# Optimization experiments

Measured on AMD Instinct MI355X. Metric: run time of the kernel, lower is better.

Reference implementation:

```python
import jax, jax.numpy as jnp
import numpy as np

B, T, D, H = 4, 1024, 1024, 16
DH = D // H
NEG_BIG = jnp.float32(-2.0**32 + 1)


def layer_norm(x, scale, bias, eps=1e-5):
    mean = jnp.mean(x, axis=-1, keepdims=True)
    var = jnp.mean(jnp.square(x - mean), axis=-1, keepdims=True)
    return (x - mean) * jax.lax.rsqrt(var + eps) * scale + bias


def setup_inputs() -> dict:
    key = jax.random.key(0)
    ks = jax.random.split(key, 10)
    s = 0.02
    x = jax.random.normal(ks[0], (B, T, D), jnp.float32)
    mask = jax.random.randint(ks[1], (B, T), 0, 2).astype(jnp.float32)
    return {
        "x": x,
        "mask": mask,
        "wq": jax.random.normal(ks[2], (D, D), jnp.float32) * s,
        "wk": jax.random.normal(ks[3], (D, D), jnp.float32) * s,
        "wv": jax.random.normal(ks[4], (D, D), jnp.float32) * s,
        "w1": jax.random.normal(ks[5], (D, D), jnp.float32) * s,
        "b1": jnp.zeros((D,), jnp.float32),
        "w2": jax.random.normal(ks[6], (D, D), jnp.float32) * s,
        "b2": jnp.zeros((D,), jnp.float32),
        "ln1_s": jnp.ones((D,), jnp.float32),
        "ln1_b": jnp.zeros((D,), jnp.float32),
        "ln2_s": jnp.ones((D,), jnp.float32),
        "ln2_b": jnp.zeros((D,), jnp.float32),
        "ln3_s": jnp.ones((D,), jnp.float32),
        "ln3_b": jnp.zeros((D,), jnp.float32),
    }


def _mask_enc(x, mask, wq, wk, wv, w1, b1, w2, b2,
              ln1_s, ln1_b, ln2_s, ln2_b, ln3_s, ln3_b):
    b, t, d = x.shape
    # --- multi-head attention (hand-rolled, matches torch split/cat trick) ---
    Q = (x @ wq).reshape(b, t, H, DH).transpose(0, 2, 1, 3)  # [B,H,T,dh]
    K = (x @ wk).reshape(b, t, H, DH).transpose(0, 2, 1, 3)
    V = (x @ wv).reshape(b, t, H, DH).transpose(0, 2, 1, 3)
    scores = jnp.einsum('bhqd,bhkd->bhqk', Q, K) / jnp.sqrt(jnp.float32(DH))
    # key padding mask from sign of |K| row sums
    key_m = jnp.sign(jnp.sum(jnp.abs(K), axis=-1))  # [B,H,T]
    scores = jnp.where(key_m[:, :, None, :] == 0, NEG_BIG, scores)
    # FORWARD direction: allowed where col_index > row_index (strict)
    idx = jnp.arange(t)
    allowed = (idx[None, :] > idx[:, None]).astype(scores.dtype)  # [T,T]
    scores = scores + (1.0 - allowed) * (-10000.0)
    attn = jax.nn.softmax(scores, axis=-1)
    # post-softmax query mask multiply
    query_m = jnp.sign(jnp.sum(jnp.abs(Q), axis=-1))[:, :, :, None]  # [B,H,T,1]
    attn = attn * query_m
    out = jnp.einsum('bhqk,bhkd->bhqd', attn, V)
    out = out.transpose(0, 2, 1, 3).reshape(b, t, d)  # combine heads
    out = out * mask[:, :, None]
    # --- residual + layernorm wrapper (attention) ---
    h1 = layer_norm(x + out, ln1_s, ln1_b)
    # --- FFN + residual + layernorm ---
    ffn = jax.nn.relu(h1 @ w1 + b1) @ w2 + b2
    h2 = layer_norm(h1 + ffn, ln2_s, ln2_b)
    # --- output normalization ---
    return layer_norm(h2, ln3_s, ln3_b)


def reference(x, mask, wq, wk, wv, w1, b1, w2, b2,
              ln1_s, ln1_b, ln2_s, ln2_b, ln3_s, ln3_b):
    return _mask_enc(x, mask, wq, wk, wv, w1, b1, w2, b2,
                     ln1_s, ln1_b, ln2_s, ln2_b, ln3_s, ln3_b)
```

## Files before the change

### kernel.cpp

```cpp
#include <hip/hip_runtime.h>
#include <stdint.h>


#define B_  4
#define T_  1024
#define D_  1024
#define H_  16
#define DH_ 64

typedef __attribute__((ext_vector_type(8))) short short8;
typedef __attribute__((ext_vector_type(4))) float floatx4;
typedef __attribute__((ext_vector_type(4))) _Float16 half4;

__device__ __forceinline__ unsigned short f2bf(float f) {
  union { float f; uint32_t u; } a; a.f = f;
  uint32_t r = a.u + 0x7FFFu + ((a.u >> 16) & 1u);
  return (unsigned short)(r >> 16);
}
__device__ __forceinline__ float bf2f(unsigned short u) {
  union { uint32_t u; float f; } a; a.u = ((uint32_t)u) << 16;
  return a.f;
}

#define GLD_LDS16(g, l) __builtin_amdgcn_global_load_lds( \
    (const __attribute__((address_space(1))) unsigned int*)(g), \
    (__attribute__((address_space(3))) unsigned int*)(l), 16, 0, 0)

__global__ __launch_bounds__(256)
void prep_kernel(const float4* __restrict__ x4, unsigned short* __restrict__ xb,
                 const float* __restrict__ w0, const float* __restrict__ w1,
                 const float* __restrict__ w2, const float* __restrict__ w3,
                 const float* __restrict__ w4, unsigned short* __restrict__ dst_all) {
  const int t = threadIdx.x;
  if (blockIdx.x < 4096) {
    int idx = blockIdx.x * 256 + t;
    float4 v = x4[idx];
    union { uint2 u; unsigned short s[4]; } o;
    o.s[0] = f2bf(v.x); o.s[1] = f2bf(v.y); o.s[2] = f2bf(v.z); o.s[3] = f2bf(v.w);
    *(uint2*)&xb[(size_t)idx * 4] = o.u;
    return;
  }
  const int b = blockIdx.x - 4096;
  const int z = b >> 8, ky = (b >> 4) & 15, nx = b & 15;
  const float* src = (z == 0) ? w0 : (z == 1) ? w1 : (z == 2) ? w2 : (z == 3) ? w3 : w4;
  unsigned short* dst = dst_all + (size_t)z * D_ * D_;
  __shared__ __align__(16) unsigned short tile[64 * 72];
  const int k0 = ky * 64, n0 = nx * 64;
#pragma unroll
  for (int c = 0; c < 4; ++c) {
    int idx = c * 256 + t;
    int r = idx >> 4, cc = (idx & 15) << 2;
    float4 v = *(const float4*)&src[(size_t)(k0 + r) * D_ + n0 + cc];
    tile[(cc + 0) * 72 + r] = f2bf(v.x);
    tile[(cc + 1) * 72 + r] = f2bf(v.y);
    tile[(cc + 2) * 72 + r] = f2bf(v.z);
    tile[(cc + 3) * 72 + r] = f2bf(v.w);
  }
  __syncthreads();
  int rr = t >> 2, ck = (t & 3) << 4;
  uint4 v0 = *(const uint4*)&tile[rr * 72 + ck];
  uint4 v1 = *(const uint4*)&tile[rr * 72 + ck + 8];
  *(uint4*)&dst[(size_t)(n0 + rr) * D_ + k0 + ck] = v0;
  *(uint4*)&dst[(size_t)(n0 + rr) * D_ + k0 + ck + 8] = v1;
}

__global__ __launch_bounds__(256, 2)
void gemm_qkv(const unsigned short* __restrict__ A,
              const unsigned short* __restrict__ Bt,
              unsigned short* __restrict__ oQ, unsigned short* __restrict__ oK,
              _Float16* __restrict__ oV) {
  const int K = 1024;
  __shared__ __align__(16) unsigned short As[128 * 32];
  __shared__ __align__(16) unsigned short Bs[128 * 32];
  __shared__ __align__(16) _Float16 Cs[2 * 64 * 136];
  const int t = threadIdx.x;
  const int lane = t & 63, w = t >> 6;
  const int quad = lane >> 4, lm = lane & 15;
  const int wm = w >> 1, wn = w & 1;
  const int m0 = blockIdx.y * 128, n0 = blockIdx.x * 128;
  const int arow = w * 32 + (lane >> 2), acol = (lane & 3) << 3;

  floatx4 acc[4][4];
#pragma unroll
  for (int i = 0; i < 4; ++i)
#pragma unroll
    for (int j = 0; j < 4; ++j) acc[i][j] = (floatx4){0.f, 0.f, 0.f, 0.f};

  for (int kt = 0; kt < K; kt += 32) {
    const unsigned short* ga = A + (size_t)(m0 + arow) * K + kt + acol;
    const unsigned short* gb = Bt + (size_t)(n0 + arow) * K + kt + acol;
    GLD_LDS16(ga, &As[(w * 32) * 32]);
    GLD_LDS16(ga + (size_t)16 * K, &As[(w * 32 + 16) * 32]);
    GLD_LDS16(gb, &Bs[(w * 32) * 32]);
    GLD_LDS16(gb + (size_t)16 * K, &Bs[(w * 32 + 16) * 32]);
    __syncthreads();
    short8 a[4], b[4];
#pragma unroll
    for (int i = 0; i < 4; ++i) a[i] = *(const short8*)&As[(wm * 64 + i * 16 + lm) * 32 + quad * 8];
#pragma unroll
    for (int j = 0; j < 4; ++j) b[j] = *(const short8*)&Bs[(wn * 64 + j * 16 + lm) * 32 + quad * 8];
#pragma unroll
    for (int i = 0; i < 4; ++i)
#pragma unroll
      for (int j = 0; j < 4; ++j)
        acc[i][j] = __builtin_amdgcn_mfma_f32_16x16x32_bf16(a[i], b[j], acc[i][j], 0, 0, 0);
    __syncthreads();
  }

  if (n0 < 2048) {
    unsigned short* p = (n0 < 1024) ? oQ : oK;
    const float qscale = (n0 < 1024) ? 0.18033688f : 1.0f;
#pragma unroll
    for (int i = 0; i < 4; ++i) {
      int gmb = m0 + wm * 64 + i * 16 + quad * 4;
#pragma unroll
      for (int j = 0; j < 4; ++j) {
        int gn = n0 + wn * 64 + j * 16 + lm;
        int nn = gn & 1023, hh = nn >> 6, dd = nn & 63;
#pragma unroll
        for (int r = 0; r < 4; ++r) {
          int gm = gmb + r;
          int bb = gm >> 10, tt = gm & 1023;
          p[(((size_t)bb * H_ + hh) * T_ + tt) * DH_ + dd] = f2bf(acc[i][j][r] * qscale);
        }
      }
    }
  } else {
#pragma unroll
    for (int i = 0; i < 4; ++i) {
#pragma unroll
      for (int j = 0; j < 4; ++j) {
        int gn = n0 + wn * 64 + j * 16 + lm;
        int hd = (gn >> 6) & 1, dd = gn & 63;
        int kperm = quad * 32 + (wm * 4 + i) * 4;
        union { _Float16 h[4]; uint2 u; } pk;
#pragma unroll
        for (int r = 0; r < 4; ++r) pk.h[r] = (_Float16)acc[i][j][r];
        *(uint2*)&Cs[((size_t)(hd * 64 + dd)) * 136 + kperm] = pk.u;
      }
    }
    __syncthreads();
    const int row = t >> 1, half = t & 1;
    const int hd = row >> 6, dd = row & 63;
    const int hh = ((n0 & 1023) >> 6) + hd;
    const int bb = m0 >> 10, kbg = (m0 >> 7) & 7;
    const _Float16* srcp = &Cs[(size_t)(hd * 64 + dd) * 136 + half * 64];
    _Float16* dstp = oV + ((((size_t)bb * H_ + hh) * DH_ + dd) * 8 + kbg) * 128 + half * 64;
#pragma unroll
    for (int g = 0; g < 8; ++g)
      *(uint4*)(dstp + g * 8) = *(const uint4*)(srcp + g * 8);
  }
}

template <int MODE>
__global__ __launch_bounds__(256, 2)
void gemm_ffn(const unsigned short* __restrict__ A,
              const unsigned short* __restrict__ Bt,
              unsigned short* __restrict__ oBf, float* __restrict__ oF,
              const float* __restrict__ bias) {
  const int K = 1024, N = 1024;
  __shared__ __align__(16) unsigned short As[64 * 32];
  __shared__ __align__(16) unsigned short Bs[128 * 32];
  const int t = threadIdx.x;
  const int lane = t & 63, w = t >> 6;
  const int quad = lane >> 4, lm = lane & 15;
  const int wm = w >> 1, wn = w & 1;
  const int m0 = blockIdx.y * 64, n0 = blockIdx.x * 128;
  const int lrow = lane >> 2, lcol = (lane & 3) << 3;

  floatx4 acc[2][4];
#pragma unroll
  for (int i = 0; i < 2; ++i)
#pragma unroll
    for (int j = 0; j < 4; ++j) acc[i][j] = (floatx4){0.f, 0.f, 0.f, 0.f};

  for (int kt = 0; kt < K; kt += 32) {
    const unsigned short* ga = A + (size_t)(m0 + w * 16 + lrow) * K + kt + lcol;
    const unsigned short* gb = Bt + (size_t)(n0 + w * 32 + lrow) * K + kt + lcol;
    GLD_LDS16(ga, &As[(w * 16) * 32]);
    GLD_LDS16(gb, &Bs[(w * 32) * 32]);
    GLD_LDS16(gb + (size_t)16 * K, &Bs[(w * 32 + 16) * 32]);
    __syncthreads();
    short8 a[2], b[4];
#pragma unroll
    for (int i = 0; i < 2; ++i) a[i] = *(const short8*)&As[(wm * 32 + i * 16 + lm) * 32 + quad * 8];
#pragma unroll
    for (int j = 0; j < 4; ++j) b[j] = *(const short8*)&Bs[(wn * 64 + j * 16 + lm) * 32 + quad * 8];
#pragma unroll
    for (int i = 0; i < 2; ++i)
#pragma unroll
      for (int j = 0; j < 4; ++j)
        acc[i][j] = __builtin_amdgcn_mfma_f32_16x16x32_bf16(a[i], b[j], acc[i][j], 0, 0, 0);
    __syncthreads();
  }

#pragma unroll
  for (int i = 0; i < 2; ++i) {
    int gmb = m0 + wm * 32 + i * 16 + quad * 4;
#pragma unroll
    for (int j = 0; j < 4; ++j) {
      int gn = n0 + wn * 64 + j * 16 + lm;
      float bv = bias[gn];
#pragma unroll
      for (int r = 0; r < 4; ++r) {
        int gm = gmb + r;
        float v = acc[i][j][r] + bv;
        if (MODE == 1) {
          oBf[(size_t)gm * N + gn] = f2bf(fmaxf(v, 0.f));
        } else {
          oF[(size_t)gm * N + gn] = v;
        }
      }
    }
  }
}

__global__ __launch_bounds__(256)
void flash_attn(const unsigned short* __restrict__ Qb,
                const unsigned short* __restrict__ Kb,
                const _Float16* __restrict__ Vtg,
                const float* __restrict__ maskp,
                unsigned short* __restrict__ attn) {
  __shared__ __align__(16) unsigned short KLs[2][8192];
  __shared__ __align__(16) _Float16      VLs[2][8192];

  const int t = threadIdx.x;
  const int lane = t & 63, w = t >> 6;
  const int quad = lane >> 4, lm = lane & 15;

  const int bid = blockIdx.x;
  const int hi  = bid >> 8;
  const int lo  = bid & 255;
  const int xcd = lo & 7;
  const int hgrp = (lo >> 3) & 7;
  const int qpair = lo >> 6;
  const int qb = hi ? (7 - qpair) : qpair;
  const int head = hgrp * 8 + xcd;
  const int hh = head & 15, bb = head >> 4;
  const int q0 = qb << 7;

  const size_t headoff = ((size_t)bb * H_ + hh) * T_ * DH_;
  const unsigned short* Qh = Qb + headoff;
  const unsigned short* Kh = Kb + headoff;
  const _Float16* Vh = Vtg + headoff;

  short8 qf[2][2];
#pragma unroll
  for (int qg = 0; qg < 2; ++qg)
#pragma unroll
    for (int ks = 0; ks < 2; ++ks)
      qf[qg][ks] = *(const short8*)(Qh + (size_t)(q0 + w * 32 + qg * 16 + lm) * 64 + ks * 32 + quad * 8);

  float lsum[2] = {0.f, 0.f};
  floatx4 acc[2][4];
#pragma unroll
  for (int qg = 0; qg < 2; ++qg)
#pragma unroll
    for (int j2 = 0; j2 < 4; ++j2) acc[qg][j2] = (floatx4){0.f, 0.f, 0.f, 0.f};

  const int qglob0 = q0 + w * 32 + lm;
  const bool excl1 = (qglob0 + 16 == 1023);
  const float MSHIFT = 14426.950408f;

  const int my_lo  = (qb == 7 && w == 3) ? 0 : qb;
  const int blk_lo = (qb == 7) ? 0 : qb;

  const unsigned short* gk[4];
  const _Float16* gv[4];
#pragma unroll
  for (int i = 0; i < 4; ++i) {
    int s = w * 4 + i;
    gk[i] = Kh + (size_t)((s >> 1) * 16 + lm) * 64 + (s & 1) * 32 + quad * 8;
    gv[i] = Vh + ((size_t)((s >> 2) * 16 + lm) * 8) * 128 + quad * 32 + (s & 3) * 8;
  }

#pragma unroll
  for (int i = 0; i < 4; ++i) {
    int s = w * 4 + i;
    GLD_LDS16(gk[i] + (size_t)blk_lo * 8192, &KLs[0][s * 512]);
    GLD_LDS16(gv[i] + (size_t)blk_lo * 128,  &VLs[0][s * 512]);
  }

  int cur = 0;
  for (int kb = blk_lo; kb < 8; ++kb) {
    __syncthreads();
    if (kb + 1 < 8) {
      int nxt = cur ^ 1;
#pragma unroll
      for (int i = 0; i < 4; ++i) {
        int s = w * 4 + i;
        GLD_LDS16(gk[i] + (size_t)(kb + 1) * 8192, &KLs[nxt][s * 512]);
        GLD_LDS16(gv[i] + (size_t)(kb + 1) * 128,  &VLs[nxt][s * 512]);
      }
    }
    if (kb >= my_lo) {
      const unsigned short* Kc = &KLs[cur][0];
      const _Float16* Vc = &VLs[cur][0];
      const int k0 = kb * 128;
      const bool need_mask = (kb <= qb);

      short8 kA = *(const short8*)&Kc[(0 * 64 + lane) * 8];
      short8 kB = *(const short8*)&Kc[(1 * 64 + lane) * 8];
      half4 vA0 = *(const half4*)&Vc[((0 * 4 + 0) * 64 + lane) * 8];
      half4 vA1 = *(const half4*)&Vc[((1 * 4 + 0) * 64 + lane) * 8];
      half4 vA2 = *(const half4*)&Vc[((2 * 4 + 0) * 64 + lane) * 8];
      half4 vA3 = *(const half4*)&Vc[((3 * 4 + 0) * 64 + lane) * 8];

#pragma unroll
      for (int j = 0; j < 8; ++j) {
        short8 nA, nB; half4 n0, n1, n2, n3;
        if (j < 7) {
          int jn = j + 1;
          nA = *(const short8*)&Kc[((jn * 2 + 0) * 64 + lane) * 8];
          nB = *(const short8*)&Kc[((jn * 2 + 1) * 64 + lane) * 8];
          n0 = *(const half4*)&Vc[((0 * 4 + (jn >> 1)) * 64 + lane) * 8 + (jn & 1) * 4];
          n1 = *(const half4*)&Vc[((1 * 4 + (jn >> 1)) * 64 + lane) * 8 + (jn & 1) * 4];
          n2 = *(const half4*)&Vc[((2 * 4 + (jn >> 1)) * 64 + lane) * 8 + (jn & 1) * 4];
          n3 = *(const half4*)&Vc[((3 * 4 + (jn >> 1)) * 64 + lane) * 8 + (jn & 1) * 4];
        }
        floatx4 st[2];
#pragma unroll
        for (int qg = 0; qg < 2; ++qg) {
          floatx4 z = (floatx4){0.f, 0.f, 0.f, 0.f};
          z = __builtin_amdgcn_mfma_f32_16x16x32_bf16(kA, qf[qg][0], z, 0, 0, 0);
          st[qg] = __builtin_amdgcn_mfma_f32_16x16x32_bf16(kB, qf[qg][1], z, 0, 0, 0);
        }
        half4 pa[2];
#pragma unroll
        for (int qg = 0; qg < 2; ++qg) {
          const int qq = qglob0 + qg * 16;
          const bool skip = (qg == 1) && excl1;
#pragma unroll
          for (int r = 0; r < 4; ++r) {
            int kg = k0 + j * 16 + quad * 4 + r;
            float v = st[qg][r];
            if (need_mask && !skip && kg <= qq) v -= MSHIFT;
            float p = __builtin_amdgcn_exp2f(v);
            lsum[qg] += p;
            pa[qg][r] = (_Float16)p;
          }
        }
        acc[0][0] = __builtin_amdgcn_mfma_f32_16x16x16f16(pa[0], vA0, acc[0][0], 0, 0, 0);
        acc[1][0] = __builtin_amdgcn_mfma_f32_16x16x16f16(pa[1], vA0, acc[1][0], 0, 0, 0);
        acc[0][1] = __builtin_amdgcn_mfma_f32_16x16x16f16(pa[0], vA1, acc[0][1], 0, 0, 0);
        acc[1][1] = __builtin_amdgcn_mfma_f32_16x16x16f16(pa[1], vA1, acc[1][1], 0, 0, 0);
        acc[0][2] = __builtin_amdgcn_mfma_f32_16x16x16f16(pa[0], vA2, acc[0][2], 0, 0, 0);
        acc[1][2] = __builtin_amdgcn_mfma_f32_16x16x16f16(pa[1], vA2, acc[1][2], 0, 0, 0);
        acc[0][3] = __builtin_amdgcn_mfma_f32_16x16x16f16(pa[0], vA3, acc[0][3], 0, 0, 0);
        acc[1][3] = __builtin_amdgcn_mfma_f32_16x16x16f16(pa[1], vA3, acc[1][3], 0, 0, 0);
        kA = nA; kB = nB; vA0 = n0; vA1 = n1; vA2 = n2; vA3 = n3;
      }
    }
    cur ^= 1;
  }

#pragma unroll
  for (int qg = 0; qg < 2; ++qg) {
    float l = lsum[qg];
    l += __shfl_xor(l, 16);
    l += __shfl_xor(l, 32);
    float s = maskp[bb * T_ + qglob0 + qg * 16] / l;
#pragma unroll
    for (int r = 0; r < 4; ++r) {
      float bsc = __shfl(s, quad * 4 + r);
      int tq = q0 + w * 32 + qg * 16 + quad * 4 + r;
#pragma unroll
      for (int j2 = 0; j2 < 4; ++j2)
        attn[((size_t)(bb * T_ + tq)) * D_ + hh * 64 + j2 * 16 + lm] = f2bf(acc[qg][j2][r] * bsc);
    }
  }
}

__global__ __launch_bounds__(256)
void ln_res_kernel(const float* __restrict__ xa, const unsigned short* __restrict__ attn,
                   const float* __restrict__ sc, const float* __restrict__ bi,
                   float* __restrict__ h, unsigned short* __restrict__ hb) {
  const int row = blockIdx.x, t = threadIdx.x;
  const int lane = t & 63, wid = t >> 6;
  size_t base = (size_t)row * D_ + t * 4;
  float4 a = *(const float4*)&xa[base];
  union { uint2 u; unsigned short s[4]; } au;
  au.u = *(const uint2*)&attn[base];
  float v0 = a.x + bf2f(au.s[0]), v1 = a.y + bf2f(au.s[1]);
  float v2 = a.z + bf2f(au.s[2]), v3 = a.w + bf2f(au.s[3]);
  float s1 = v0 + v1 + v2 + v3;
  float s2 = v0 * v0 + v1 * v1 + v2 * v2 + v3 * v3;
#pragma unroll
  for (int off = 32; off; off >>= 1) { s1 += __shfl_down(s1, off); s2 += __shfl_down(s2, off); }
  __shared__ float r1[4], r2[4];
  if (lane == 0) { r1[wid] = s1; r2[wid] = s2; }
  __syncthreads();
  s1 = r1[0] + r1[1] + r1[2] + r1[3];
  s2 = r2[0] + r2[1] + r2[2] + r2[3];
  float mean = s1 * (1.f / 1024.f);
  float var = s2 * (1.f / 1024.f) - mean * mean;
  float rstd = rsqrtf(var + 1e-5f);
  float4 sv = *(const float4*)&sc[t * 4];
  float4 bv = *(const float4*)&bi[t * 4];
  float o0 = (v0 - mean) * rstd * sv.x + bv.x;
  float o1 = (v1 - mean) * rstd * sv.y + bv.y;
  float o2 = (v2 - mean) * rstd * sv.z + bv.z;
  float o3 = (v3 - mean) * rstd * sv.w + bv.w;
  float4 ov = {o0, o1, o2, o3};
  *(float4*)&h[base] = ov;
  union { uint2 u; unsigned short s[4]; } ob;
  ob.s[0] = f2bf(o0); ob.s[1] = f2bf(o1); ob.s[2] = f2bf(o2); ob.s[3] = f2bf(o3);
  *(uint2*)&hb[base] = ob.u;
}

__global__ __launch_bounds__(256)
void ln_double_kernel(const float* __restrict__ h1, const float* __restrict__ ffn,
                      const float* __restrict__ s2c, const float* __restrict__ b2c,
                      const float* __restrict__ s3c, const float* __restrict__ b3c,
                      float* __restrict__ out) {
  const int row = blockIdx.x, t = threadIdx.x;
  const int lane = t & 63, wid = t >> 6;
  size_t base = (size_t)row * D_ + t * 4;
  float4 a = *(const float4*)&h1[base];
  float4 b = *(const float4*)&ffn[base];
  float v0 = a.x + b.x, v1 = a.y + b.y, v2 = a.z + b.z, v3 = a.w + b.w;
  float s1 = v0 + v1 + v2 + v3;
  float s2 = v0 * v0 + v1 * v1 + v2 * v2 + v3 * v3;
#pragma unroll
  for (int off = 32; off; off >>= 1) { s1 += __shfl_down(s1, off); s2 += __shfl_down(s2, off); }
  __shared__ float ra[4], rb[4], rc[4], rd[4];
  if (lane == 0) { ra[wid] = s1; rb[wid] = s2; }
  __syncthreads();
  s1 = ra[0] + ra[1] + ra[2] + ra[3];
  s2 = rb[0] + rb[1] + rb[2] + rb[3];
  float mean = s1 * (1.f / 1024.f);
  float var = s2 * (1.f / 1024.f) - mean * mean;
  float rstd = rsqrtf(var + 1e-5f);
  float4 sv = *(const float4*)&s2c[t * 4];
  float4 bv = *(const float4*)&b2c[t * 4];
  float o0 = (v0 - mean) * rstd * sv.x + bv.x;
  float o1 = (v1 - mean) * rstd * sv.y + bv.y;
  float o2 = (v2 - mean) * rstd * sv.z + bv.z;
  float o3 = (v3 - mean) * rstd * sv.w + bv.w;
  float u1 = o0 + o1 + o2 + o3;
  float u2 = o0 * o0 + o1 * o1 + o2 * o2 + o3 * o3;
#pragma unroll
  for (int off = 32; off; off >>= 1) { u1 += __shfl_down(u1, off); u2 += __shfl_down(u2, off); }
  if (lane == 0) { rc[wid] = u1; rd[wid] = u2; }
  __syncthreads();
  u1 = rc[0] + rc[1] + rc[2] + rc[3];
  u2 = rd[0] + rd[1] + rd[2] + rd[3];
  float mean2 = u1 * (1.f / 1024.f);
  float var2 = u2 * (1.f / 1024.f) - mean2 * mean2;
  float rstd2 = rsqrtf(var2 + 1e-5f);
  float4 s3v = *(const float4*)&s3c[t * 4];
  float4 b3v = *(const float4*)&b3c[t * 4];
  float4 fo;
  fo.x = (o0 - mean2) * rstd2 * s3v.x + b3v.x;
  fo.y = (o1 - mean2) * rstd2 * s3v.y + b3v.y;
  fo.z = (o2 - mean2) * rstd2 * s3v.z + b3v.z;
  fo.w = (o3 - mean2) * rstd2 * s3v.w + b3v.w;
  *(float4*)&out[base] = fo;
}

extern "C" void kernel_launch(void* const* d_in, const int* in_sizes, int n_in,
                              void* d_out, int out_size, void* d_ws, size_t ws_size,
                              hipStream_t stream) {
  (void)in_sizes; (void)n_in; (void)out_size; (void)ws_size;
  const float* x   = (const float*)d_in[0];
  const float* msk = (const float*)d_in[1];
  const float* wq  = (const float*)d_in[2];
  const float* wk  = (const float*)d_in[3];
  const float* wv  = (const float*)d_in[4];
  const float* w1  = (const float*)d_in[5];
  const float* b1  = (const float*)d_in[6];
  const float* w2  = (const float*)d_in[7];
  const float* b2  = (const float*)d_in[8];
  const float* l1s = (const float*)d_in[9];
  const float* l1b = (const float*)d_in[10];
  const float* l2s = (const float*)d_in[11];
  const float* l2b = (const float*)d_in[12];
  const float* l3s = (const float*)d_in[13];
  const float* l3b = (const float*)d_in[14];
  float* outp = (float*)d_out;

  char* ws = (char*)d_ws;
  unsigned short* xb   = (unsigned short*)(ws);
  unsigned short* wt   = (unsigned short*)(ws + ((size_t)8  << 20));
  unsigned short* Qb   = (unsigned short*)(ws + ((size_t)18 << 20));
  unsigned short* Kb   = (unsigned short*)(ws + ((size_t)26 << 20));
  _Float16*       Vtg  = (_Float16*)(ws + ((size_t)34 << 20));
  unsigned short* attn = (unsigned short*)(ws + ((size_t)42 << 20));
  float* h1            = (float*)(ws + ((size_t)50 << 20));
  unsigned short* h1b  = (unsigned short*)(ws + ((size_t)18 << 20));
  unsigned short* gb   = (unsigned short*)(ws + ((size_t)26 << 20));
  float* ffn           = (float*)(ws + ((size_t)34 << 20));

  prep_kernel<<<4096 + 1280, 256, 0, stream>>>((const float4*)x, xb,
                                               wq, wk, wv, w1, w2, wt);
  gemm_qkv<<<dim3(24, 32), 256, 0, stream>>>(xb, wt, Qb, Kb, Vtg);
  flash_attn<<<512, 256, 0, stream>>>(Qb, Kb, Vtg, msk, attn);
  ln_res_kernel<<<4096, 256, 0, stream>>>(x, attn, l1s, l1b, h1, h1b);
  gemm_ffn<1><<<dim3(8, 64), 256, 0, stream>>>(h1b, wt + (size_t)3 * 1024 * 1024, gb, nullptr, b1);
  gemm_ffn<2><<<dim3(8, 64), 256, 0, stream>>>(gb, wt + (size_t)4 * 1024 * 1024, nullptr, ffn, b2);
  ln_double_kernel<<<4096, 256, 0, stream>>>(h1, ffn, l2s, l2b, l3s, l3b, outp);
}
```

Baseline: 235.1 us.

## Store FFN output in bf16, use one wave per row in layernorms, batch x conversion

The second FFN GEMM now writes its output as bf16 instead of fp32, which halves that intermediate's write and read traffic, and the final layernorm kernel reads the bf16 version. Both layernorm kernels switch from one 256-thread block per row to one wavefront per row with 16 elements per lane. The row reductions then use only xor shuffles, with no shared memory or __syncthreads, and each block covers four rows. The x-to-bf16 conversion in the prep kernel now processes four float4 per thread across a quarter as many blocks. Rounding the FFN output to bf16 before the residual add and layernorm adds precision loss.

```diff
diff --git a/kernel.cpp b/kernel.cpp
--- a/kernel.cpp
+++ b/kernel.cpp
@@ -32,15 +32,19 @@
                  const float* __restrict__ w2, const float* __restrict__ w3,
                  const float* __restrict__ w4, unsigned short* __restrict__ dst_all) {
   const int t = threadIdx.x;
-  if (blockIdx.x < 4096) {
-    int idx = blockIdx.x * 256 + t;
-    float4 v = x4[idx];
-    union { uint2 u; unsigned short s[4]; } o;
-    o.s[0] = f2bf(v.x); o.s[1] = f2bf(v.y); o.s[2] = f2bf(v.z); o.s[3] = f2bf(v.w);
-    *(uint2*)&xb[(size_t)idx * 4] = o.u;
+  if (blockIdx.x < 1024) {
+    int idx0 = blockIdx.x * 1024 + t;
+#pragma unroll
+    for (int c = 0; c < 4; ++c) {
+      int idx = idx0 + c * 256;
+      float4 v = x4[idx];
+      union { uint2 u; unsigned short s[4]; } o;
+      o.s[0] = f2bf(v.x); o.s[1] = f2bf(v.y); o.s[2] = f2bf(v.z); o.s[3] = f2bf(v.w);
+      *(uint2*)&xb[(size_t)idx * 4] = o.u;
+    }
     return;
   }
-  const int b = blockIdx.x - 4096;
+  const int b = blockIdx.x - 1024;
   const int z = b >> 8, ky = (b >> 4) & 15, nx = b & 15;
   const float* src = (z == 0) ? w0 : (z == 1) ? w1 : (z == 2) ? w2 : (z == 3) ? w3 : w4;
   unsigned short* dst = dst_all + (size_t)z * D_ * D_;
@@ -156,7 +160,7 @@
 __global__ __launch_bounds__(256, 2)
 void gemm_ffn(const unsigned short* __restrict__ A,
               const unsigned short* __restrict__ Bt,
-              unsigned short* __restrict__ oBf, float* __restrict__ oF,
+              unsigned short* __restrict__ oBf,
               const float* __restrict__ bias) {
   const int K = 1024, N = 1024;
   __shared__ __align__(16) unsigned short As[64 * 32];
@@ -205,11 +209,8 @@
       for (int r = 0; r < 4; ++r) {
         int gm = gmb + r;
         float v = acc[i][j][r] + bv;
-        if (MODE == 1) {
-          oBf[(size_t)gm * N + gn] = f2bf(fmaxf(v, 0.f));
-        } else {
-          oF[(size_t)gm * N + gn] = v;
-        }
+        if (MODE == 1) v = fmaxf(v, 0.f);
+        oBf[(size_t)gm * N + gn] = f2bf(v);
       }
     }
   }
@@ -375,87 +376,117 @@
 void ln_res_kernel(const float* __restrict__ xa, const unsigned short* __restrict__ attn,
                    const float* __restrict__ sc, const float* __restrict__ bi,
                    float* __restrict__ h, unsigned short* __restrict__ hb) {
-  const int row = blockIdx.x, t = threadIdx.x;
-  const int lane = t & 63, wid = t >> 6;
-  size_t base = (size_t)row * D_ + t * 4;
-  float4 a = *(const float4*)&xa[base];
-  union { uint2 u; unsigned short s[4]; } au;
-  au.u = *(const uint2*)&attn[base];
-  float v0 = a.x + bf2f(au.s[0]), v1 = a.y + bf2f(au.s[1]);
-  float v2 = a.z + bf2f(au.s[2]), v3 = a.w + bf2f(au.s[3]);
-  float s1 = v0 + v1 + v2 + v3;
-  float s2 = v0 * v0 + v1 * v1 + v2 * v2 + v3 * v3;
-#pragma unroll
-  for (int off = 32; off; off >>= 1) { s1 += __shfl_down(s1, off); s2 += __shfl_down(s2, off); }
-  __shared__ float r1[4], r2[4];
-  if (lane == 0) { r1[wid] = s1; r2[wid] = s2; }
-  __syncthreads();
-  s1 = r1[0] + r1[1] + r1[2] + r1[3];
-  s2 = r2[0] + r2[1] + r2[2] + r2[3];
+  const int t = threadIdx.x;
+  const int lane = t & 63, w = t >> 6;
+  const int row = blockIdx.x * 4 + w;
+  const size_t base = (size_t)row * D_ + lane * 16;
+
+  float v[16];
+  float s1 = 0.f, s2 = 0.f;
+#pragma unroll
+  for (int i = 0; i < 4; ++i) {
+    float4 a = *(const float4*)&xa[base + i * 4];
+    union { uint2 u; unsigned short s[4]; } au;
+    au.u = *(const uint2*)&attn[base + i * 4];
+    float x0 = a.x + bf2f(au.s[0]);
+    float x1 = a.y + bf2f(au.s[1]);
+    float x2 = a.z + bf2f(au.s[2]);
+    float x3 = a.w + bf2f(au.s[3]);
+    v[i * 4 + 0] = x0; v[i * 4 + 1] = x1; v[i * 4 + 2] = x2; v[i * 4 + 3] = x3;
+    s1 += x0 + x1 + x2 + x3;
+    s2 += x0 * x0 + x1 * x1 + x2 * x2 + x3 * x3;
+  }
+#pragma unroll
+  for (int off = 1; off < 64; off <<= 1) {
+    s1 += __shfl_xor(s1, off);
+    s2 += __shfl_xor(s2, off);
+  }
   float mean = s1 * (1.f / 1024.f);
   float var = s2 * (1.f / 1024.f) - mean * mean;
   float rstd = rsqrtf(var + 1e-5f);
-  float4 sv = *(const float4*)&sc[t * 4];
-  float4 bv = *(const float4*)&bi[t * 4];
-  float o0 = (v0 - mean) * rstd * sv.x + bv.x;
-  float o1 = (v1 - mean) * rstd * sv.y + bv.y;
-  float o2 = (v2 - mean) * rstd * sv.z + bv.z;
-  float o3 = (v3 - mean) * rstd * sv.w + bv.w;
-  float4 ov = {o0, o1, o2, o3};
-  *(float4*)&h[base] = ov;
-  union { uint2 u; unsigned short s[4]; } ob;
-  ob.s[0] = f2bf(o0); ob.s[1] = f2bf(o1); ob.s[2] = f2bf(o2); ob.s[3] = f2bf(o3);
-  *(uint2*)&hb[base] = ob.u;
+#pragma unroll
+  for (int i = 0; i < 4; ++i) {
+    float4 sv = *(const float4*)&sc[lane * 16 + i * 4];
+    float4 bv = *(const float4*)&bi[lane * 16 + i * 4];
+    float o0 = (v[i * 4 + 0] - mean) * rstd * sv.x + bv.x;
+    float o1 = (v[i * 4 + 1] - mean) * rstd * sv.y + bv.y;
+    float o2 = (v[i * 4 + 2] - mean) * rstd * sv.z + bv.z;
+    float o3 = (v[i * 4 + 3] - mean) * rstd * sv.w + bv.w;
+    float4 ov = {o0, o1, o2, o3};
+    *(float4*)&h[base + i * 4] = ov;
+    union { uint2 u; unsigned short s[4]; } ob;
+    ob.s[0] = f2bf(o0); ob.s[1] = f2bf(o1); ob.s[2] = f2bf(o2); ob.s[3] = f2bf(o3);
+    *(uint2*)&hb[base + i * 4] = ob.u;
+  }
 }
 
 __global__ __launch_bounds__(256)
-void ln_double_kernel(const float* __restrict__ h1, const float* __restrict__ ffn,
+void ln_double_kernel(const float* __restrict__ h1, const unsigned short* __restrict__ ffnb,
                       const float* __restrict__ s2c, const float* __restrict__ b2c,
                       const float* __restrict__ s3c, const float* __restrict__ b3c,
                       float* __restrict__ out) {
-  const int row = blockIdx.x, t = threadIdx.x;
-  const int lane = t & 63, wid = t >> 6;
-  size_t base = (size_t)row * D_ + t * 4;
-  float4 a = *(const float4*)&h1[base];
-  float4 b = *(const float4*)&ffn[base];
-  float v0 = a.x + b.x, v1 = a.y + b.y, v2 = a.z + b.z, v3 = a.w + b.w;
-  float s1 = v0 + v1 + v2 + v3;
-  float s2 = v0 * v0 + v1 * v1 + v2 * v2 + v3 * v3;
-#pragma unroll
-  for (int off = 32; off; off >>= 1) { s1 += __shfl_down(s1, off); s2 += __shfl_down(s2, off); }
-  __shared__ float ra[4], rb[4], rc[4], rd[4];
-  if (lane == 0) { ra[wid] = s1; rb[wid] = s2; }
-  __syncthreads();
-  s1 = ra[0] + ra[1] + ra[2] + ra[3];
-  s2 = rb[0] + rb[1] + rb[2] + rb[3];
+  const int t = threadIdx.x;
+  const int lane = t & 63, w = t >> 6;
+  const int row = blockIdx.x * 4 + w;
+  const size_t base = (size_t)row * D_ + lane * 16;
+
+  float v[16];
+  float s1 = 0.f, s2 = 0.f;
+#pragma unroll
+  for (int i = 0; i < 4; ++i) {
+    float4 a = *(const float4*)&h1[base + i * 4];
+    union { uint2 u; unsigned short s[4]; } fu;
+    fu.u = *(const uint2*)&ffnb[base + i * 4];
+    float x0 = a.x + bf2f(fu.s[0]);
+    float x1 = a.y + bf2f(fu.s[1]);
+    float x2 = a.z + bf2f(fu.s[2]);
+    float x3 = a.w + bf2f(fu.s[3]);
+    v[i * 4 + 0] = x0; v[i * 4 + 1] = x1; v[i * 4 + 2] = x2; v[i * 4 + 3] = x3;
+    s1 += x0 + x1 + x2 + x3;
+    s2 += x0 * x0 + x1 * x1 + x2 * x2 + x3 * x3;
+  }
+#pragma unroll
+  for (int off = 1; off < 64; off <<= 1) {
+    s1 += __shfl_xor(s1, off);
+    s2 += __shfl_xor(s2, off);
+  }
   float mean = s1 * (1.f / 1024.f);
   float var = s2 * (1.f / 1024.f) - mean * mean;
   float rstd = rsqrtf(var + 1e-5f);
-  float4 sv = *(const float4*)&s2c[t * 4];
-  float4 bv = *(const float4*)&b2c[t * 4];
-  float o0 = (v0 - mean) * rstd * sv.x + bv.x;
-  float o1 = (v1 - mean) * rstd * sv.y + bv.y;
-  float o2 = (v2 - mean) * rstd * sv.z + bv.z;
-  float o3 = (v3 - mean) * rstd * sv.w + bv.w;
-  float u1 = o0 + o1 + o2 + o3;
-  float u2 = o0 * o0 + o1 * o1 + o2 * o2 + o3 * o3;
-#pragma unroll
-  for (int off = 32; off; off >>= 1) { u1 += __shfl_down(u1, off); u2 += __shfl_down(u2, off); }
-  if (lane == 0) { rc[wid] = u1; rd[wid] = u2; }
-  __syncthreads();
-  u1 = rc[0] + rc[1] + rc[2] + rc[3];
-  u2 = rd[0] + rd[1] + rd[2] + rd[3];
+
+  float o[16];
+  float u1 = 0.f, u2 = 0.f;
+#pragma unroll
+  for (int i = 0; i < 4; ++i) {
+    float4 sv = *(const float4*)&s2c[lane * 16 + i * 4];
+    float4 bv = *(const float4*)&b2c[lane * 16 + i * 4];
+    float o0 = (v[i * 4 + 0] - mean) * rstd * sv.x + bv.x;
+    float o1 = (v[i * 4 + 1] - mean) * rstd * sv.y + bv.y;
+    float o2 = (v[i * 4 + 2] - mean) * rstd * sv.z + bv.z;
+    float o3 = (v[i * 4 + 3] - mean) * rstd * sv.w + bv.w;
+    o[i * 4 + 0] = o0; o[i * 4 + 1] = o1; o[i * 4 + 2] = o2; o[i * 4 + 3] = o3;
+    u1 += o0 + o1 + o2 + o3;
+    u2 += o0 * o0 + o1 * o1 + o2 * o2 + o3 * o3;
+  }
+#pragma unroll
+  for (int off = 1; off < 64; off <<= 1) {
+    u1 += __shfl_xor(u1, off);
+    u2 += __shfl_xor(u2, off);
+  }
   float mean2 = u1 * (1.f / 1024.f);
   float var2 = u2 * (1.f / 1024.f) - mean2 * mean2;
   float rstd2 = rsqrtf(var2 + 1e-5f);
-  float4 s3v = *(const float4*)&s3c[t * 4];
-  float4 b3v = *(const float4*)&b3c[t * 4];
-  float4 fo;
-  fo.x = (o0 - mean2) * rstd2 * s3v.x + b3v.x;
-  fo.y = (o1 - mean2) * rstd2 * s3v.y + b3v.y;
-  fo.z = (o2 - mean2) * rstd2 * s3v.z + b3v.z;
-  fo.w = (o3 - mean2) * rstd2 * s3v.w + b3v.w;
-  *(float4*)&out[base] = fo;
+#pragma unroll
+  for (int i = 0; i < 4; ++i) {
+    float4 sv = *(const float4*)&s3c[lane * 16 + i * 4];
+    float4 bv = *(const float4*)&b3c[lane * 16 + i * 4];
+    float4 fo;
+    fo.x = (o[i * 4 + 0] - mean2) * rstd2 * sv.x + bv.x;
+    fo.y = (o[i * 4 + 1] - mean2) * rstd2 * sv.y + bv.y;
+    fo.z = (o[i * 4 + 2] - mean2) * rstd2 * sv.z + bv.z;
+    fo.w = (o[i * 4 + 3] - mean2) * rstd2 * sv.w + bv.w;
+    *(float4*)&out[base + i * 4] = fo;
+  }
 }
 
 extern "C" void kernel_launch(void* const* d_in, const int* in_sizes, int n_in,
@@ -489,14 +520,14 @@
   float* h1            = (float*)(ws + ((size_t)50 << 20));
   unsigned short* h1b  = (unsigned short*)(ws + ((size_t)18 << 20));
   unsigned short* gb   = (unsigned short*)(ws + ((size_t)26 << 20));
-  float* ffn           = (float*)(ws + ((size_t)34 << 20));
-
-  prep_kernel<<<4096 + 1280, 256, 0, stream>>>((const float4*)x, xb,
+  unsigned short* ffnb = (unsigned short*)(ws + ((size_t)34 << 20));
+
+  prep_kernel<<<1024 + 1280, 256, 0, stream>>>((const float4*)x, xb,
                                                wq, wk, wv, w1, w2, wt);
   gemm_qkv<<<dim3(24, 32), 256, 0, stream>>>(xb, wt, Qb, Kb, Vtg);
   flash_attn<<<512, 256, 0, stream>>>(Qb, Kb, Vtg, msk, attn);
-  ln_res_kernel<<<4096, 256, 0, stream>>>(x, attn, l1s, l1b, h1, h1b);
-  gemm_ffn<1><<<dim3(8, 64), 256, 0, stream>>>(h1b, wt + (size_t)3 * 1024 * 1024, gb, nullptr, b1);
-  gemm_ffn<2><<<dim3(8, 64), 256, 0, stream>>>(gb, wt + (size_t)4 * 1024 * 1024, nullptr, ffn, b2);
-  ln_double_kernel<<<4096, 256, 0, stream>>>(h1, ffn, l2s, l2b, l3s, l3b, outp);
-}
+  ln_res_kernel<<<1024, 256, 0, stream>>>(x, attn, l1s, l1b, h1, h1b);
+  gemm_ffn<1><<<dim3(8, 64), 256, 0, stream>>>(h1b, wt + (size_t)3 * 1024 * 1024, gb, b1);
+  gemm_ffn<2><<<dim3(8, 64), 256, 0, stream>>>(gb, wt + (size_t)4 * 1024 * 1024, ffnb, b2);
+  ln_double_kernel<<<1024, 256, 0, stream>>>(h1, ffnb, l2s, l2b, l3s, l3b, outp);
+}
```

Result: no change. 236.4 us (+0.5%).
